# Kernel tuning notes

Measured on AMD Instinct MI355X. Metric: run time of the kernel, lower is better.

## Reference

```python
import jax, jax.numpy as jnp
import numpy as np

B, N, H, DH, ORDER, DEG = 64, 256, 8, 64, 4, 16
D = H * DH
TOTAL = B * N
E = TOTAL * DEG


def setup_inputs() -> dict:
    key = jax.random.key(0)
    ks = jax.random.split(key, 16)
    output = jax.random.normal(ks[0], (N, B, D), dtype=jnp.float32)
    # attention weights: positive, row-normalized like softmax output
    attn = jax.nn.softmax(jax.random.normal(ks[1], (B, H, N, N), dtype=jnp.float32), axis=-1)
    out_each_head = jax.random.normal(ks[2], (B, N, H, DH), dtype=jnp.float32)
    # random graph edges, endpoints within the same graph (global node ids)
    g = jax.random.randint(ks[3], (E,), 0, B)
    s = g * N + jax.random.randint(ks[4], (E,), 0, N)
    d = g * N + jax.random.randint(ks[5], (E,), 0, N)
    edge_index = jnp.stack([s, d], axis=0).astype(jnp.int64)
    # full graphs, no padding: feature_indices[:,0]=graph id, [:,1]=node pos
    fi = jnp.stack([jnp.repeat(jnp.arange(B), N), jnp.tile(jnp.arange(N), B)], axis=1).astype(jnp.int64)
    batch = fi[:, 0]
    sc = 0.1
    params = dict(
        W_gcn=jax.random.normal(ks[6], (ORDER, ORDER)) * sc,
        b_gcn=jnp.zeros((ORDER,), jnp.float32),
        W_lin=jax.random.normal(ks[7], (ORDER, ORDER)) * sc,
        b_lin=jnp.zeros((ORDER,), jnp.float32),
        W_cheb=jax.random.normal(ks[8], (ORDER, DH, DH)) * sc,
        b_cheb=jnp.zeros((DH,), jnp.float32),
        W_cat=jax.random.normal(ks[9], (2 * D, D)) * sc,
        b_cat=jnp.zeros((D,), jnp.float32),
        gamma=jnp.ones((D,), jnp.float32),
        beta=jnp.zeros((D,), jnp.float32),
    )
    return dict(output=output, attn=attn, out_each_head=out_each_head,
                edge_index=edge_index, feature_indices=fi, batch=batch, **params)


def reference(output, attn, out_each_head, edge_index, feature_indices, batch,
              W_gcn, b_gcn, W_lin, b_lin, W_cheb, b_cheb, W_cat, b_cat, gamma, beta):
    Bn, Hn, Nn, _ = attn.shape
    C = W_gcn.shape[0]
    total = Bn * Nn
    NT = Hn * total

    # ---- get_filter_coefficients: GCN over fully-connected attention graphs ----
    # edge weights are detached in the original (edge_weight.detach())
    A = jax.lax.stop_gradient(attn).transpose(1, 0, 2, 3).reshape(Hn * Bn, Nn, Nn)
    A_hat = A + jnp.eye(Nn, dtype=A.dtype)  # add self loops (weight 1)
    deg = A_hat.sum(axis=1)                 # deg_j = sum_i A_hat[i,j]
    dinv = jnp.where(deg > 0, jax.lax.rsqrt(deg), 0.0)  # (HB, N)
    # x = ones, so x @ W_gcn is a constant row = column sums of W_gcn
    w_row = W_gcn.sum(axis=0)               # (C,)
    s = jnp.einsum('bi,bij->bj', dinv, A_hat) * dinv     # (HB, N)
    x_c = jnp.tanh(s[:, :, None] * w_row + b_gcn)        # (HB, N, C)
    gap = x_c.mean(axis=1)                  # global avg pool per graph (HB, C)
    coeff = gap @ W_lin + b_lin             # (HB, C) rows ordered (head, batch)

    # ---- dynamic Chebyshev filtering per head on the input graph ----
    offsets = (jnp.arange(Hn) * total).astype(edge_index.dtype)
    src = (edge_index[0][None, :] + offsets[:, None]).reshape(-1)
    dst = (edge_index[1][None, :] + offsets[:, None]).reshape(-1)
    deg_n = jax.ops.segment_sum(jnp.ones(src.shape[0], jnp.float32), dst, num_segments=NT)
    dinv_n = jnp.where(deg_n > 0, jax.lax.rsqrt(deg_n), 0.0)
    norm_e = -(dinv_n[src] * dinv_n[dst])   # scaled Laplacian L_hat = -D^-1/2 A D^-1/2

    def prop(x):  # L_hat @ x via gather/scatter
        return jax.ops.segment_sum(norm_e[:, None] * x[src], dst, num_segments=NT)

    # nodes ordered (head, batch, node)
    x0 = out_each_head.transpose(2, 0, 1, 3).reshape(NT, DH)
    batch_all = (batch[None, :] + (jnp.arange(Hn) * Bn)[:, None]).reshape(-1)  # graph id h*B+b
    c_node = coeff[batch_all]               # (NT, ORDER) per-node dynamic coefficients

    T_prev, T_cur = x0, prop(x0)
    acc = c_node[:, 0:1] * (T_prev @ W_cheb[0]) + c_node[:, 1:2] * (T_cur @ W_cheb[1])
    for k in range(2, C):
        T_next = 2.0 * prop(T_cur) - T_prev
        acc = acc + c_node[:, k:k + 1] * (T_next @ W_cheb[k])
        T_prev, T_cur = T_cur, T_next
    acc = acc + b_cheb                      # (NT, DH)

    # regroup heads: (H, B*N, DH) -> (B*N, H*DH), scatter back to (N, B, D)
    filtered = acc.reshape(Hn, total, DH).transpose(1, 0, 2).reshape(total, Hn * DH)
    out_filtered = jnp.zeros_like(output).at[feature_indices[:, 1], feature_indices[:, 0], :].set(filtered)

    # skip connection + linear_cat + final LayerNorm
    out_cat = jnp.concatenate([output, out_filtered], axis=-1)
    out = out_cat @ W_cat + b_cat
    mu = out.mean(axis=-1, keepdims=True)
    var = ((out - mu) ** 2).mean(axis=-1, keepdims=True)
    out = (out - mu) * jax.lax.rsqrt(var + 1e-5) * gamma + beta
    return out
```

## Files before the change

kernel.cpp:

```cpp
#include <hip/hip_runtime.h>
#include <stdint.h>

#define Bq      64
#define Nq      256
#define Hq      8
#define DHq     64
#define TOTALq  16384
#define NTq     131072
#define Dq      512

typedef __attribute__((ext_vector_type(8))) short short8;
typedef __attribute__((ext_vector_type(4))) float floatx4;

__device__ __forceinline__ unsigned short f2bf(float f) {
    union { float f; unsigned int u; } c; c.f = f;
    unsigned int u = c.u;
    return (unsigned short)((u + 0x7fffu + ((u >> 16) & 1u)) >> 16);
}
__device__ __forceinline__ float bf2f(unsigned short u) {
    union { unsigned int u; float f; } c; c.u = ((unsigned int)u) << 16;
    return c.f;
}


__global__ void count_deg_kernel(const int* __restrict__ dstp, int* __restrict__ cnt, int E) {
    int e = blockIdx.x * 256 + threadIdx.x;
    if (e < E) atomicAdd(&cnt[dstp[e]], 1);
}

__global__ void dinv_kernel(const int* __restrict__ cnt, float* __restrict__ dinv_n) {
    int v = blockIdx.x * 256 + threadIdx.x;
    if (v < TOTALq) {
        int c = cnt[v];
        dinv_n[v] = (c > 0) ? rsqrtf((float)c) : 0.0f;
    }
}

__global__ void pscatter_kernel(const int* __restrict__ srcp, const int* __restrict__ dstp,
                                const float* __restrict__ dinv_n, float* __restrict__ Pf, int E) {
    int e = blockIdx.x * 256 + threadIdx.x;
    if (e >= E) return;
    int s = srcp[e], d = dstp[e];
    int g = d >> 8;
    atomicAdd(&Pf[((size_t)g << 16) + ((size_t)(d & 255) << 8) + (s & 255)],
              -(dinv_n[s] * dinv_n[d]));
}

__global__ void pconv_kernel(const float* __restrict__ Pf, unsigned short* __restrict__ Pb) {
    int i = (blockIdx.x * 256 + threadIdx.x) * 4;
    float4 v = *(const float4*)(Pf + i);
    unsigned int lo = (unsigned int)f2bf(v.x) | ((unsigned int)f2bf(v.y) << 16);
    unsigned int hi = (unsigned int)f2bf(v.z) | ((unsigned int)f2bf(v.w) << 16);
    *(uint2*)(Pb + i) = make_uint2(lo, hi);
}

__global__ void x0t_kernel(const float* __restrict__ X, unsigned short* __restrict__ Xt) {
    __shared__ float tile[64 * 68];
    int t = threadIdx.x;
    int n0 = blockIdx.x * 64, c0 = blockIdx.y * 64;
#pragma unroll
    for (int it = 0; it < 4; ++it) {
        int idx = it * 256 + t;
        int nr = idx >> 4, sub = idx & 15;
        float4 v = *(const float4*)(X + (size_t)(n0 + nr) * 512 + c0 + sub * 4);
        *(float4*)(&tile[nr * 68 + sub * 4]) = v;
    }
    __syncthreads();
#pragma unroll
    for (int it = 0; it < 2; ++it) {
        int idx = it * 256 + t;
        int cr = idx >> 3, sub = idx & 7;
        unsigned int pk[4];
#pragma unroll
        for (int q = 0; q < 4; ++q) {
            unsigned short a = f2bf(tile[(sub * 8 + q * 2 + 0) * 68 + cr]);
            unsigned short b = f2bf(tile[(sub * 8 + q * 2 + 1) * 68 + cr]);
            pk[q] = (unsigned int)a | ((unsigned int)b << 16);
        }
        *(uint4*)(Xt + (size_t)(c0 + cr) * 16384 + n0 + sub * 8) =
            make_uint4(pk[0], pk[1], pk[2], pk[3]);
    }
}

__global__ void wchebt_kernel(const float* __restrict__ W, float* __restrict__ WT) {
    int idx = blockIdx.x * 256 + threadIdx.x;
    int k = idx >> 12, rem = idx & 4095;
    int n = rem >> 6, j = rem & 63;
    WT[idx] = W[(k << 12) + (j << 6) + n];
}

__global__ __launch_bounds__(512)
void coeff_kernel(const float* __restrict__ attn,
                  const float* __restrict__ Wg, const float* __restrict__ bg,
                  const float* __restrict__ Wlin, const float* __restrict__ blin,
                  float* __restrict__ coeff) {
    __shared__ floatx4 part[8][64];
    __shared__ floatx4 dinv4[64];
    const int g = blockIdx.x;
    const int h = g >> 6;
    const int b = g & 63;
    const float* A = attn + ((size_t)(b * Hq + h)) * (Nq * Nq);
    const int tid = threadIdx.x;
    const int rg = tid >> 6;
    const int cv = tid & 63;
    const float* Ap = A + cv * 4;

    floatx4 s1 = (floatx4){0.f, 0.f, 0.f, 0.f};
#pragma unroll 8
    for (int r = 0; r < 32; ++r)
        s1 += *(const floatx4*)(Ap + (size_t)(rg * 32 + r) * 256);
    part[rg][cv] = s1;
    __syncthreads();

    if (tid < 64) {
        floatx4 cs = part[0][tid];
#pragma unroll
        for (int i = 1; i < 8; ++i) cs += part[i][tid];
        floatx4 dv;
#pragma unroll
        for (int i = 0; i < 4; ++i) dv[i] = rsqrtf(cs[i] + 1.0f);
        dinv4[tid] = dv;
    }
    __syncthreads();

    const float* dsc = (const float*)dinv4;
    floatx4 s2 = (floatx4){0.f, 0.f, 0.f, 0.f};
#pragma unroll 8
    for (int r = 0; r < 32; ++r) {
        int rr = rg * 32 + r;
        s2 += dsc[rr] * (*(const floatx4*)(Ap + (size_t)rr * 256));
    }
    part[rg][cv] = s2;
    __syncthreads();

    if (tid < 64) {
        floatx4 ws = part[0][tid];
#pragma unroll
        for (int i = 1; i < 8; ++i) ws += part[i][tid];
        floatx4 dv = dinv4[tid];
        floatx4 sj = (ws + dv) * dv;

        float wr[4], bgl[4];
#pragma unroll
        for (int c = 0; c < 4; ++c) {
            wr[c]  = Wg[0 * 4 + c] + Wg[1 * 4 + c] + Wg[2 * 4 + c] + Wg[3 * 4 + c];
            bgl[c] = bg[c];
        }
        float v[4];
#pragma unroll
        for (int c = 0; c < 4; ++c) {
            v[c] = tanhf(sj[0] * wr[c] + bgl[c]) + tanhf(sj[1] * wr[c] + bgl[c]) +
                   tanhf(sj[2] * wr[c] + bgl[c]) + tanhf(sj[3] * wr[c] + bgl[c]);
#pragma unroll
            for (int o = 32; o >= 1; o >>= 1) v[c] += __shfl_down(v[c], o, 64);
        }
        float g0 = __shfl(v[0], 0, 64), g1 = __shfl(v[1], 0, 64);
        float g2 = __shfl(v[2], 0, 64), g3 = __shfl(v[3], 0, 64);
        if (tid < 4) {
            float r = blin[tid] + (g0 * Wlin[0 * 4 + tid] + g1 * Wlin[1 * 4 + tid] +
                                   g2 * Wlin[2 * 4 + tid] + g3 * Wlin[3 * 4 + tid]) *
                                      (1.0f / 256.0f);
            coeff[g * 4 + tid] = r;
        }
    }
}

__global__ __launch_bounds__(256, 2)
void cheb_prop(const unsigned short* __restrict__ Pb,
               const unsigned short* __restrict__ Tc,
               const unsigned short* __restrict__ Tp,
               unsigned short* __restrict__ Tn, int first) {
    __shared__ unsigned short A_lds[128 * 40];
    __shared__ unsigned short B_lds[128 * 40];
    const int b = blockIdx.x, mb = blockIdx.y, cb = blockIdx.z;
    const int tid = threadIdx.x, lane = tid & 63, wv = tid >> 6;
    const int wr = wv & 1, wc = wv >> 1, quad = lane >> 4, l15 = lane & 15;
    const unsigned short* Pbase = Pb + ((size_t)b << 16) + (size_t)mb * 128 * 256;

    floatx4 acc[4][4];
#pragma unroll
    for (int rt = 0; rt < 4; ++rt)
#pragma unroll
        for (int ct = 0; ct < 4; ++ct) acc[rt][ct] = (floatx4){0.f, 0.f, 0.f, 0.f};

    for (int kt = 0; kt < 8; ++kt) {
        const int kc = kt * 32;
        __syncthreads();
#pragma unroll
        for (int it = 0; it < 2; ++it) {
            int idx = it * 256 + tid;
            int row = idx >> 2, sub = idx & 3;
            *(uint4*)(A_lds + row * 40 + sub * 8) =
                *(const uint4*)(Pbase + row * 256 + kc + sub * 8);
            *(uint4*)(B_lds + row * 40 + sub * 8) =
                *(const uint4*)(Tc + (size_t)(cb * 128 + row) * 16384 + b * 256 + kc + sub * 8);
        }
        __syncthreads();
        short8 af[4], bfr[4];
#pragma unroll
        for (int rt = 0; rt < 4; ++rt)
            af[rt] = *(const short8*)(A_lds + (wr * 64 + rt * 16 + l15) * 40 + quad * 8);
#pragma unroll
        for (int ct = 0; ct < 4; ++ct)
            bfr[ct] = *(const short8*)(B_lds + (wc * 64 + ct * 16 + l15) * 40 + quad * 8);
#pragma unroll
        for (int rt = 0; rt < 4; ++rt)
#pragma unroll
            for (int ct = 0; ct < 4; ++ct)
                acc[rt][ct] = __builtin_amdgcn_mfma_f32_16x16x32_bf16(af[rt], bfr[ct],
                                                                     acc[rt][ct], 0, 0, 0);
    }
#pragma unroll
    for (int rt = 0; rt < 4; ++rt)
#pragma unroll
        for (int ct = 0; ct < 4; ++ct) {
            int col = cb * 128 + wc * 64 + ct * 16 + l15;
            int m = mb * 128 + wr * 64 + rt * 16 + quad * 4;
            size_t base = (size_t)col * 16384 + b * 256 + m;
            float v[4];
            if (first) {
#pragma unroll
                for (int i = 0; i < 4; ++i) v[i] = acc[rt][ct][i];
            } else {
                uint2 tp = *(const uint2*)(Tp + base);
                v[0] = 2.0f * acc[rt][ct][0] - bf2f((unsigned short)(tp.x & 0xffff));
                v[1] = 2.0f * acc[rt][ct][1] - bf2f((unsigned short)(tp.x >> 16));
                v[2] = 2.0f * acc[rt][ct][2] - bf2f((unsigned short)(tp.y & 0xffff));
                v[3] = 2.0f * acc[rt][ct][3] - bf2f((unsigned short)(tp.y >> 16));
            }
            unsigned int lo = (unsigned int)f2bf(v[0]) | ((unsigned int)f2bf(v[1]) << 16);
            unsigned int hi = (unsigned int)f2bf(v[2]) | ((unsigned int)f2bf(v[3]) << 16);
            *(uint2*)(Tn + base) = make_uint2(lo, hi);
        }
}

__global__ __launch_bounds__(256, 2)
void filt_kernel(const float* __restrict__ oeh,
                 const unsigned short* __restrict__ T1t, const unsigned short* __restrict__ T2t,
                 const unsigned short* __restrict__ T3t, const float* __restrict__ WchTf,
                 const float* __restrict__ coeff, const float* __restrict__ bch,
                 unsigned short* __restrict__ filtb) {
    __shared__ unsigned short A_lds[256 * 72];
    __shared__ unsigned short W_lds[64 * 72];
    const int b = blockIdx.x, h = blockIdx.y;
    const int tid = threadIdx.x, lane = tid & 63, wv = tid >> 6;
    const int quad = lane >> 4, l15 = lane & 15;

    floatx4 acc[4][4];
#pragma unroll
    for (int rt = 0; rt < 4; ++rt)
#pragma unroll
        for (int ct = 0; ct < 4; ++ct) acc[rt][ct] = (floatx4){0.f, 0.f, 0.f, 0.f};

    for (int k = 0; k < 4; ++k) {
        float ck = coeff[(h * Bq + b) * 4 + k];
        __syncthreads();
        if (k == 0) {
#pragma unroll
            for (int it = 0; it < 8; ++it) {
                int idx = it * 256 + tid;
                int row = idx >> 3, sub = idx & 7;
                const float* sp = oeh + (size_t)(b * 256 + row) * 512 + h * 64 + sub * 8;
                float4 v0 = *(const float4*)sp;
                float4 v1 = *(const float4*)(sp + 4);
                unsigned int p0 = (unsigned int)f2bf(v0.x) | ((unsigned int)f2bf(v0.y) << 16);
                unsigned int p1 = (unsigned int)f2bf(v0.z) | ((unsigned int)f2bf(v0.w) << 16);
                unsigned int p2 = (unsigned int)f2bf(v1.x) | ((unsigned int)f2bf(v1.y) << 16);
                unsigned int p3 = (unsigned int)f2bf(v1.z) | ((unsigned int)f2bf(v1.w) << 16);
                *(uint4*)(A_lds + row * 72 + ((sub ^ ((row >> 3) & 7)) << 3)) =
                    make_uint4(p0, p1, p2, p3);
            }
        } else {
            const unsigned short* Tk = (k == 1) ? T1t : (k == 2) ? T2t : T3t;
            const unsigned short* base = Tk + (size_t)(h * 64) * 16384 + b * 256;
#pragma unroll
            for (int it = 0; it < 4; ++it) {
                int idx = it * 256 + tid;
                int cr2 = idx >> 5;
                int nch = idx & 31;
                int n0 = nch * 8;
                int crA = cr2 * 2;
                uint4 a  = *(const uint4*)(base + (size_t)crA * 16384 + n0);
                uint4 c4 = *(const uint4*)(base + (size_t)(crA + 1) * 16384 + n0);
                unsigned swz = (unsigned)((((crA >> 3) ^ (nch & 7)) << 3) + (crA & 7));
                unsigned short* dst = A_lds + swz;
                unsigned av[4] = {a.x, a.y, a.z, a.w};
                unsigned cv4[4] = {c4.x, c4.y, c4.z, c4.w};
#pragma unroll
                for (int w2 = 0; w2 < 4; ++w2) {
                    unsigned lo = (av[w2] & 0xffffu) | (cv4[w2] << 16);
                    unsigned hi = (av[w2] >> 16) | (cv4[w2] & 0xffff0000u);
                    *(unsigned*)(dst + (n0 + w2 * 2 + 0) * 72) = lo;
                    *(unsigned*)(dst + (n0 + w2 * 2 + 1) * 72) = hi;
                }
            }
        }
#pragma unroll
        for (int it = 0; it < 2; ++it) {
            int idx = it * 256 + tid;
            int r = idx >> 3, sub = idx & 7;
            const float* wp = WchTf + k * 4096 + r * 64 + sub * 8;
            float4 w0 = *(const float4*)wp;
            float4 w1 = *(const float4*)(wp + 4);
            unsigned int p0 = (unsigned int)f2bf(w0.x * ck) | ((unsigned int)f2bf(w0.y * ck) << 16);
            unsigned int p1 = (unsigned int)f2bf(w0.z * ck) | ((unsigned int)f2bf(w0.w * ck) << 16);
            unsigned int p2 = (unsigned int)f2bf(w1.x * ck) | ((unsigned int)f2bf(w1.y * ck) << 16);
            unsigned int p3 = (unsigned int)f2bf(w1.z * ck) | ((unsigned int)f2bf(w1.w * ck) << 16);
            *(uint4*)(W_lds + r * 72 + sub * 8) = make_uint4(p0, p1, p2, p3);
        }
        __syncthreads();
#pragma unroll
        for (int kk = 0; kk < 2; ++kk) {
            short8 af[4], bfr[4];
#pragma unroll
            for (int rt = 0; rt < 4; ++rt) {
                int node = wv * 64 + rt * 16 + l15;
                int blk = ((kk << 2) + quad) ^ ((node >> 3) & 7);
                af[rt] = *(const short8*)(A_lds + node * 72 + (blk << 3));
            }
#pragma unroll
            for (int ct = 0; ct < 4; ++ct)
                bfr[ct] = *(const short8*)(W_lds + (ct * 16 + l15) * 72 + kk * 32 + quad * 8);
#pragma unroll
            for (int rt = 0; rt < 4; ++rt)
#pragma unroll
                for (int ct = 0; ct < 4; ++ct)
                    acc[rt][ct] = __builtin_amdgcn_mfma_f32_16x16x32_bf16(af[rt], bfr[ct],
                                                                         acc[rt][ct], 0, 0, 0);
        }
    }
#pragma unroll
    for (int rt = 0; rt < 4; ++rt)
#pragma unroll
        for (int ct = 0; ct < 4; ++ct) {
            int coln = ct * 16 + l15;
            float bias = bch[coln];
#pragma unroll
            for (int i = 0; i < 4; ++i) {
                int m = wv * 64 + rt * 16 + quad * 4 + i;
                size_t r = (size_t)m * 64 + b;
                filtb[r * 512 + h * 64 + coln] = f2bf(acc[rt][ct][i] + bias);
            }
        }
}

__global__ void wt2_kernel(const float* __restrict__ W, unsigned short* __restrict__ Wt2) {
    int idx = blockIdx.x * 256 + threadIdx.x;
    int col = idx & 511;
    int ktq = idx >> 9;
    const float* src = W + (size_t)(ktq * 8) * 512 + col;
    unsigned int pk[4];
#pragma unroll
    for (int q2 = 0; q2 < 4; ++q2) {
        unsigned short a = f2bf(src[(q2 * 2 + 0) * 512]);
        unsigned short b = f2bf(src[(q2 * 2 + 1) * 512]);
        pk[q2] = (unsigned int)a | ((unsigned int)b << 16);
    }
    *(uint4*)(Wt2 + (size_t)idx * 8) = make_uint4(pk[0], pk[1], pk[2], pk[3]);
}

__global__ __launch_bounds__(512, 2)
void gemm_ln_mfma(const float* __restrict__ outp, const unsigned short* __restrict__ filtb,
                  const unsigned short* __restrict__ Wt2, const float* __restrict__ bcat,
                  const float* __restrict__ gamma, const float* __restrict__ beta,
                  float* __restrict__ out) {
    extern __shared__ unsigned char smc[];
    unsigned short* A_lds0 = (unsigned short*)smc;
    unsigned short* A_lds1 = (unsigned short*)(smc + 4096);
    float* ep = (float*)smc;

    const int tid = threadIdx.x;
    const int lane = tid & 63;
    const int wv = tid >> 6;
    const int quad = lane >> 4;
    const int l15 = lane & 15;
    const int r0 = blockIdx.x * 64;

    const int s_row = tid >> 3;
    const int s_sub = tid & 7;
    const int s_q   = s_sub >> 1;
    const int s_e   = (s_sub & 1) * 4;

    const size_t boff = (size_t)(quad * 512 + wv * 64 + l15) * 8;

    floatx4 acc[4][4];
#pragma unroll
    for (int rt = 0; rt < 4; ++rt)
#pragma unroll
        for (int ct = 0; ct < 4; ++ct) acc[rt][ct] = (floatx4){0.f, 0.f, 0.f, 0.f};

    short8 bA[4], bB[4];

    {
#pragma unroll
        for (int ct = 0; ct < 4; ++ct)
            bA[ct] = *(const short8*)(Wt2 + boff + ct * 128);
        float4 av = *(const float4*)(outp + (size_t)(r0 + s_row) * 512 + s_sub * 4);
        uint2 ap;
        ap.x = (unsigned int)f2bf(av.x) | ((unsigned int)f2bf(av.y) << 16);
        ap.y = (unsigned int)f2bf(av.z) | ((unsigned int)f2bf(av.w) << 16);
        *(uint2*)(A_lds0 + (s_q * 64 + s_row) * 8 + s_e) = ap;
        __syncthreads();
    }

#define GSTEP(KT, BC, BN, AC, AN, HASNEXT)                                          \
    do {                                                                            \
        const int kt_ = (KT);                                                       \
        const bool hn_ = (HASNEXT);                                                 \
        const bool isf_ = (kt_ + 1 < 16);                                           \
        float4 av_; uint2 afb_;                                                     \
        if (hn_) {                                                                  \
            _Pragma("unroll")                                                       \
            for (int ct = 0; ct < 4; ++ct)                                          \
                BN[ct] = *(const short8*)(Wt2 + (size_t)(kt_ + 1) * 16384 +         \
                                          boff + ct * 128);                         \
            const int kc_ = (kt_ + 1) * 32;                                         \
            if (isf_)                                                               \
                av_ = *(const float4*)(outp + (size_t)(r0 + s_row) * 512 +          \
                                       kc_ + s_sub * 4);                            \
            else                                                                    \
                afb_ = *(const uint2*)(filtb + (size_t)(r0 + s_row) * 512 +         \
                                       (kc_ - 512) + s_sub * 4);                    \
        }                                                                           \
        short8 af_[4];                                                              \
        _Pragma("unroll")                                                           \
        for (int rt = 0; rt < 4; ++rt)                                              \
            af_[rt] = *(const short8*)(AC + (quad * 64 + rt * 16 + l15) * 8);       \
        _Pragma("unroll")                                                           \
        for (int rt = 0; rt < 4; ++rt)                                              \
            _Pragma("unroll")                                                       \
            for (int ct = 0; ct < 4; ++ct)                                          \
                acc[rt][ct] = __builtin_amdgcn_mfma_f32_16x16x32_bf16(              \
                    af_[rt], BC[ct], acc[rt][ct], 0, 0, 0);                         \
        if (hn_) {                                                                  \
            uint2 ap_;                                                              \
            if (isf_) {                                                             \
                ap_.x = (unsigned int)f2bf(av_.x) | ((unsigned int)f2bf(av_.y) << 16); \
                ap_.y = (unsigned int)f2bf(av_.z) | ((unsigned int)f2bf(av_.w) << 16); \
            } else {                                                                \
                ap_ = afb_;                                                         \
            }                                                                       \
            *(uint2*)(AN + (s_q * 64 + s_row) * 8 + s_e) = ap_;                     \
        }                                                                           \
        __syncthreads();                                                            \
    } while (0)

    for (int kt2 = 0; kt2 < 16; ++kt2) {
        GSTEP(2 * kt2,     bA, bB, A_lds0, A_lds1, true);
        GSTEP(2 * kt2 + 1, bB, bA, A_lds1, A_lds0, kt2 < 15);
    }
#undef GSTEP

    float gg[8], bb[8];
#pragma unroll
    for (int i = 0; i < 8; ++i) { gg[i] = gamma[i * 64 + lane]; bb[i] = beta[i * 64 + lane]; }
    float bc[4];
#pragma unroll
    for (int ct = 0; ct < 4; ++ct) bc[ct] = bcat[wv * 64 + ct * 16 + l15];

    for (int half = 0; half < 2; ++half) {
        __syncthreads();
#pragma unroll
        for (int rt2 = 0; rt2 < 2; ++rt2) {
            const int rt = half * 2 + rt2;
#pragma unroll
            for (int ct = 0; ct < 4; ++ct) {
                const int col = wv * 64 + ct * 16 + l15;
#pragma unroll
                for (int i = 0; i < 4; ++i) {
                    const int row_l = rt2 * 16 + quad * 4 + i;
                    ep[row_l * 512 + col] = acc[rt][ct][i] + bc[ct];
                }
            }
        }
        __syncthreads();
#pragma unroll
        for (int m4 = 0; m4 < 4; ++m4) {
            const int m = wv * 4 + m4;
            float s = 0.0f, ss = 0.0f;
#pragma unroll
            for (int i = 0; i < 8; ++i) {
                float v = ep[m * 512 + i * 64 + lane];
                s += v; ss += v * v;
            }
#pragma unroll
            for (int o = 32; o >= 1; o >>= 1) {
                s += __shfl_down(s, o, 64);
                ss += __shfl_down(ss, o, 64);
            }
            s = __shfl(s, 0, 64);
            ss = __shfl(ss, 0, 64);
            const float mu = s * (1.0f / 512.0f);
            const float var = ss * (1.0f / 512.0f) - mu * mu;
            const float rs = rsqrtf(var + 1e-5f);
            const int r = r0 + half * 32 + m;
#pragma unroll
            for (int i = 0; i < 8; ++i) {
                const int d = i * 64 + lane;
                out[(size_t)r * 512 + d] = (ep[m * 512 + d] - mu) * rs * gg[i] + bb[i];
            }
        }
    }
}

extern "C" void kernel_launch(void* const* d_in, const int* in_sizes, int n_in,
                              void* d_out, int out_size, void* d_ws, size_t ws_size,
                              hipStream_t stream) {
    const float* output       = (const float*)d_in[0];
    const float* attn         = (const float*)d_in[1];
    const float* oeh          = (const float*)d_in[2];
    const int*   edge_index   = (const int*)d_in[3];
    const float* W_gcn        = (const float*)d_in[6];
    const float* b_gcn        = (const float*)d_in[7];
    const float* W_lin        = (const float*)d_in[8];
    const float* b_lin        = (const float*)d_in[9];
    const float* W_cheb       = (const float*)d_in[10];
    const float* b_cheb       = (const float*)d_in[11];
    const float* W_cat        = (const float*)d_in[12];
    const float* b_cat        = (const float*)d_in[13];
    const float* gamma        = (const float*)d_in[14];
    const float* beta         = (const float*)d_in[15];
    float* out = (float*)d_out;

    const int E = in_sizes[3] / 2;
    const int* srcp = edge_index;
    const int* dstp = edge_index + E;

    uint8_t* ws = (uint8_t*)d_ws;
    size_t cur = 0;
    auto alloc = [&](size_t bytes) -> void* {
        void* p = ws + cur;
        cur += (bytes + 255) & ~(size_t)255;
        return p;
    };
    int*   cnt     = (int*)alloc(TOTALq * sizeof(int));
    float* dinv_n  = (float*)alloc(TOTALq * sizeof(float));
    float* Pf      = (float*)alloc((size_t)64 * 65536 * sizeof(float));
    unsigned short* Pb   = (unsigned short*)alloc((size_t)64 * 65536 * 2);
    float* coeff   = (float*)alloc(512 * 4 * sizeof(float));
    unsigned short* X0_t = (unsigned short*)alloc((size_t)512 * 16384 * 2);
    unsigned short* T1_t = (unsigned short*)alloc((size_t)512 * 16384 * 2);
    unsigned short* T2_t = (unsigned short*)alloc((size_t)512 * 16384 * 2);
    unsigned short* T3_t = (unsigned short*)alloc((size_t)512 * 16384 * 2);
    float* WchTf   = (float*)alloc(4 * 64 * 64 * sizeof(float));
    unsigned short* Wt2  = (unsigned short*)alloc((size_t)Dq * 1024 * 2);
    unsigned short* filtb = (unsigned short*)alloc((size_t)TOTALq * Dq * 2);
    (void)ws_size; (void)n_in; (void)out_size;

    hipMemsetAsync(cnt, 0, TOTALq * sizeof(int), stream);
    count_deg_kernel<<<(E + 255) / 256, 256, 0, stream>>>(dstp, cnt, E);
    dinv_kernel<<<TOTALq / 256, 256, 0, stream>>>(cnt, dinv_n);
    hipMemsetAsync(Pf, 0, (size_t)64 * 65536 * sizeof(float), stream);
    pscatter_kernel<<<(E + 255) / 256, 256, 0, stream>>>(srcp, dstp, dinv_n, Pf, E);
    pconv_kernel<<<4096, 256, 0, stream>>>(Pf, Pb);

    x0t_kernel<<<dim3(256, 8), 256, 0, stream>>>(oeh, X0_t);
    coeff_kernel<<<Hq * Bq, 512, 0, stream>>>(attn, W_gcn, b_gcn, W_lin, b_lin, coeff);
    wt2_kernel<<<256, 256, 0, stream>>>(W_cat, Wt2);
    wchebt_kernel<<<64, 256, 0, stream>>>(W_cheb, WchTf);

    dim3 pg(64, 2, 4);
    cheb_prop<<<pg, 256, 0, stream>>>(Pb, X0_t, nullptr, T1_t, 1);
    cheb_prop<<<pg, 256, 0, stream>>>(Pb, T1_t, X0_t, T2_t, 0);
    cheb_prop<<<pg, 256, 0, stream>>>(Pb, T2_t, T1_t, T3_t, 0);

    filt_kernel<<<dim3(64, 8), 256, 0, stream>>>(oeh, T1_t, T2_t, T3_t, WchTf, coeff,
                                                 b_cheb, filtb);

    gemm_ln_mfma<<<TOTALq / 64, 512, 65536, stream>>>(output, filtb, Wt2, b_cat,
                                                      gamma, beta, out);
}
```

Baseline: 437.0 us.

## Fuse Chebyshev propagation and filter GEMM into one per-graph-head kernel

Replaces the transpose kernel, three cheb_prop launches and filt_kernel with a single kernel, one block per (head, graph). Each block keeps its 256x64 slice of T_k resident in LDS in both row- and column-major swizzled layouts. It runs the three propagation GEMMs and the coefficient-scaled W_cheb GEMM on chip, so the T1/T2/T3 intermediates never round-trip through global memory. The P operand is now read straight from global per wave rather than staged in LDS. With 512 blocks of 512 threads and about 73KB of dynamic LDS each, occupancy is reduced.

```diff
diff --git a/kernel.cpp b/kernel.cpp
--- a/kernel.cpp
+++ b/kernel.cpp
@@ -52,34 +52,6 @@
     unsigned int lo = (unsigned int)f2bf(v.x) | ((unsigned int)f2bf(v.y) << 16);
     unsigned int hi = (unsigned int)f2bf(v.z) | ((unsigned int)f2bf(v.w) << 16);
     *(uint2*)(Pb + i) = make_uint2(lo, hi);
-}
-
-__global__ void x0t_kernel(const float* __restrict__ X, unsigned short* __restrict__ Xt) {
-    __shared__ float tile[64 * 68];
-    int t = threadIdx.x;
-    int n0 = blockIdx.x * 64, c0 = blockIdx.y * 64;
-#pragma unroll
-    for (int it = 0; it < 4; ++it) {
-        int idx = it * 256 + t;
-        int nr = idx >> 4, sub = idx & 15;
-        float4 v = *(const float4*)(X + (size_t)(n0 + nr) * 512 + c0 + sub * 4);
-        *(float4*)(&tile[nr * 68 + sub * 4]) = v;
-    }
-    __syncthreads();
-#pragma unroll
-    for (int it = 0; it < 2; ++it) {
-        int idx = it * 256 + t;
-        int cr = idx >> 3, sub = idx & 7;
-        unsigned int pk[4];
-#pragma unroll
-        for (int q = 0; q < 4; ++q) {
-            unsigned short a = f2bf(tile[(sub * 8 + q * 2 + 0) * 68 + cr]);
-            unsigned short b = f2bf(tile[(sub * 8 + q * 2 + 1) * 68 + cr]);
-            pk[q] = (unsigned int)a | ((unsigned int)b << 16);
-        }
-        *(uint4*)(Xt + (size_t)(c0 + cr) * 16384 + n0 + sub * 8) =
-            make_uint4(pk[0], pk[1], pk[2], pk[3]);
-    }
 }
 
 __global__ void wchebt_kernel(const float* __restrict__ W, float* __restrict__ WT) {
@@ -165,181 +137,182 @@
     }
 }
 
-__global__ __launch_bounds__(256, 2)
-void cheb_prop(const unsigned short* __restrict__ Pb,
-               const unsigned short* __restrict__ Tc,
-               const unsigned short* __restrict__ Tp,
-               unsigned short* __restrict__ Tn, int first) {
-    __shared__ unsigned short A_lds[128 * 40];
-    __shared__ unsigned short B_lds[128 * 40];
-    const int b = blockIdx.x, mb = blockIdx.y, cb = blockIdx.z;
-    const int tid = threadIdx.x, lane = tid & 63, wv = tid >> 6;
-    const int wr = wv & 1, wc = wv >> 1, quad = lane >> 4, l15 = lane & 15;
-    const unsigned short* Pbase = Pb + ((size_t)b << 16) + (size_t)mb * 128 * 256;
-
-    floatx4 acc[4][4];
+__global__ __launch_bounds__(512, 2)
+void cheb_fused(const unsigned short* __restrict__ Pb, const float* __restrict__ oeh,
+                const float* __restrict__ WchTf, const float* __restrict__ coeff,
+                const float* __restrict__ bch, unsigned short* __restrict__ filtb) {
+    extern __shared__ unsigned char sm[];
+    unsigned short* cm = (unsigned short*)sm;
+    unsigned short* rm = (unsigned short*)(sm + 32768);
+    unsigned short* Wl = (unsigned short*)(sm + 65536);
+
+    const int g = blockIdx.x;
+    const int b = (g & 7) * 8 + ((g >> 3) & 7);
+    const int h = g >> 6;
+    const int tid = threadIdx.x;
+    const int lane = tid & 63, wv = tid >> 6;
+    const int wr = wv >> 1, wc = wv & 1;
+    const int quad = lane >> 4, l15 = lane & 15;
+
+    const unsigned short* Pbase = Pb + ((size_t)b << 16);
+    const float* cf = coeff + (h * 64 + b) * 4;
+
+    {
+        const int sn = tid >> 1;
+        const int sh = (tid & 1) * 32;
+        const float* sp = oeh + (size_t)(b * 256 + sn) * 512 + h * 64 + sh;
+        unsigned int pk[16];
+#pragma unroll
+        for (int j = 0; j < 8; ++j) {
+            float4 v = *(const float4*)(sp + j * 4);
+            pk[2 * j]     = (unsigned)f2bf(v.x) | ((unsigned)f2bf(v.y) << 16);
+            pk[2 * j + 1] = (unsigned)f2bf(v.z) | ((unsigned)f2bf(v.w) << 16);
+        }
+#pragma unroll
+        for (int jj = 0; jj < 4; ++jj)
+            *(uint4*)(rm + sn * 64 + ((((sh >> 3) + jj) ^ (sn & 7)) << 3)) =
+                make_uint4(pk[4 * jj], pk[4 * jj + 1], pk[4 * jj + 2], pk[4 * jj + 3]);
+#pragma unroll
+        for (int e = 0; e < 32; ++e) {
+            int c = sh + e;
+            unsigned short v =
+                (unsigned short)((e & 1) ? (pk[e >> 1] >> 16) : (pk[e >> 1] & 0xffffu));
+            cm[c * 256 + (((sn >> 3) ^ (c & 31)) << 3) + (sn & 7)] = v;
+        }
+        float ck = cf[0];
+        int r = tid >> 3, su = tid & 7;
+        const float* wp = WchTf + r * 64 + su * 8;
+        float4 w0 = *(const float4*)wp, w1 = *(const float4*)(wp + 4);
+        *(uint4*)(Wl + r * 72 + su * 8) = make_uint4(
+            (unsigned)f2bf(w0.x * ck) | ((unsigned)f2bf(w0.y * ck) << 16),
+            (unsigned)f2bf(w0.z * ck) | ((unsigned)f2bf(w0.w * ck) << 16),
+            (unsigned)f2bf(w1.x * ck) | ((unsigned)f2bf(w1.y * ck) << 16),
+            (unsigned)f2bf(w1.z * ck) | ((unsigned)f2bf(w1.w * ck) << 16));
+    }
+    __syncthreads();
+
+    unsigned int curp[4][2][2], prvp[4][2][2];
 #pragma unroll
     for (int rt = 0; rt < 4; ++rt)
 #pragma unroll
-        for (int ct = 0; ct < 4; ++ct) acc[rt][ct] = (floatx4){0.f, 0.f, 0.f, 0.f};
-
-    for (int kt = 0; kt < 8; ++kt) {
-        const int kc = kt * 32;
-        __syncthreads();
-#pragma unroll
-        for (int it = 0; it < 2; ++it) {
-            int idx = it * 256 + tid;
-            int row = idx >> 2, sub = idx & 3;
-            *(uint4*)(A_lds + row * 40 + sub * 8) =
-                *(const uint4*)(Pbase + row * 256 + kc + sub * 8);
-            *(uint4*)(B_lds + row * 40 + sub * 8) =
-                *(const uint4*)(Tc + (size_t)(cb * 128 + row) * 16384 + b * 256 + kc + sub * 8);
-        }
-        __syncthreads();
-        short8 af[4], bfr[4];
-#pragma unroll
-        for (int rt = 0; rt < 4; ++rt)
-            af[rt] = *(const short8*)(A_lds + (wr * 64 + rt * 16 + l15) * 40 + quad * 8);
-#pragma unroll
-        for (int ct = 0; ct < 4; ++ct)
-            bfr[ct] = *(const short8*)(B_lds + (wc * 64 + ct * 16 + l15) * 40 + quad * 8);
-#pragma unroll
-        for (int rt = 0; rt < 4; ++rt)
-#pragma unroll
-            for (int ct = 0; ct < 4; ++ct)
-                acc[rt][ct] = __builtin_amdgcn_mfma_f32_16x16x32_bf16(af[rt], bfr[ct],
-                                                                     acc[rt][ct], 0, 0, 0);
-    }
+        for (int ct = 0; ct < 2; ++ct)
+#pragma unroll
+            for (int p = 0; p < 2; ++p) {
+                int m = wr * 64 + rt * 16 + quad * 4 + 2 * p;
+                int c = wc * 32 + ct * 16 + l15;
+                curp[rt][ct][p] = *(const unsigned int*)(cm + c * 256 +
+                                                         (((m >> 3) ^ (c & 31)) << 3) + (m & 7));
+                prvp[rt][ct][p] = 0u;
+            }
+
+    floatx4 accf[4][2];
 #pragma unroll
     for (int rt = 0; rt < 4; ++rt)
 #pragma unroll
-        for (int ct = 0; ct < 4; ++ct) {
-            int col = cb * 128 + wc * 64 + ct * 16 + l15;
-            int m = mb * 128 + wr * 64 + rt * 16 + quad * 4;
-            size_t base = (size_t)col * 16384 + b * 256 + m;
-            float v[4];
-            if (first) {
-#pragma unroll
-                for (int i = 0; i < 4; ++i) v[i] = acc[rt][ct][i];
-            } else {
-                uint2 tp = *(const uint2*)(Tp + base);
-                v[0] = 2.0f * acc[rt][ct][0] - bf2f((unsigned short)(tp.x & 0xffff));
-                v[1] = 2.0f * acc[rt][ct][1] - bf2f((unsigned short)(tp.x >> 16));
-                v[2] = 2.0f * acc[rt][ct][2] - bf2f((unsigned short)(tp.y & 0xffff));
-                v[3] = 2.0f * acc[rt][ct][3] - bf2f((unsigned short)(tp.y >> 16));
-            }
-            unsigned int lo = (unsigned int)f2bf(v[0]) | ((unsigned int)f2bf(v[1]) << 16);
-            unsigned int hi = (unsigned int)f2bf(v[2]) | ((unsigned int)f2bf(v[3]) << 16);
-            *(uint2*)(Tn + base) = make_uint2(lo, hi);
-        }
-}
-
-__global__ __launch_bounds__(256, 2)
-void filt_kernel(const float* __restrict__ oeh,
-                 const unsigned short* __restrict__ T1t, const unsigned short* __restrict__ T2t,
-                 const unsigned short* __restrict__ T3t, const float* __restrict__ WchTf,
-                 const float* __restrict__ coeff, const float* __restrict__ bch,
-                 unsigned short* __restrict__ filtb) {
-    __shared__ unsigned short A_lds[256 * 72];
-    __shared__ unsigned short W_lds[64 * 72];
-    const int b = blockIdx.x, h = blockIdx.y;
-    const int tid = threadIdx.x, lane = tid & 63, wv = tid >> 6;
-    const int quad = lane >> 4, l15 = lane & 15;
-
-    floatx4 acc[4][4];
+        for (int ct = 0; ct < 2; ++ct) accf[rt][ct] = (floatx4){0.f, 0.f, 0.f, 0.f};
+
+#pragma unroll
+    for (int k = 0; k < 4; ++k) {
+#pragma unroll
+        for (int kk = 0; kk < 2; ++kk) {
+            short8 af[4], bfw[2];
+#pragma unroll
+            for (int rt = 0; rt < 4; ++rt) {
+                int row = wr * 64 + rt * 16 + l15;
+                af[rt] = *(const short8*)(rm + row * 64 + (((kk * 4 + quad) ^ (row & 7)) << 3));
+            }
+#pragma unroll
+            for (int ct = 0; ct < 2; ++ct) {
+                int oc = wc * 32 + ct * 16 + l15;
+                bfw[ct] = *(const short8*)(Wl + oc * 72 + kk * 32 + quad * 8);
+            }
+#pragma unroll
+            for (int rt = 0; rt < 4; ++rt)
+#pragma unroll
+                for (int ct = 0; ct < 2; ++ct)
+                    accf[rt][ct] = __builtin_amdgcn_mfma_f32_16x16x32_bf16(
+                        af[rt], bfw[ct], accf[rt][ct], 0, 0, 0);
+        }
+        if (k < 3) {
+            floatx4 accp[4][2];
+#pragma unroll
+            for (int rt = 0; rt < 4; ++rt)
+#pragma unroll
+                for (int ct = 0; ct < 2; ++ct) accp[rt][ct] = (floatx4){0.f, 0.f, 0.f, 0.f};
+#pragma unroll
+            for (int kt = 0; kt < 8; ++kt) {
+                short8 ap[4], bp[2];
+#pragma unroll
+                for (int rt = 0; rt < 4; ++rt) {
+                    int row = wr * 64 + rt * 16 + l15;
+                    ap[rt] = *(const short8*)(Pbase + row * 256 + kt * 32 + quad * 8);
+                }
+#pragma unroll
+                for (int ct = 0; ct < 2; ++ct) {
+                    int c = wc * 32 + ct * 16 + l15;
+                    bp[ct] = *(const short8*)(cm + c * 256 + (((kt * 4 + quad) ^ (c & 31)) << 3));
+                }
+#pragma unroll
+                for (int rt = 0; rt < 4; ++rt)
+#pragma unroll
+                    for (int ct = 0; ct < 2; ++ct)
+                        accp[rt][ct] = __builtin_amdgcn_mfma_f32_16x16x32_bf16(
+                            ap[rt], bp[ct], accp[rt][ct], 0, 0, 0);
+            }
+            __syncthreads();
+#pragma unroll
+            for (int rt = 0; rt < 4; ++rt)
+#pragma unroll
+                for (int ct = 0; ct < 2; ++ct)
+#pragma unroll
+                    for (int p = 0; p < 2; ++p) {
+                        float a0 = accp[rt][ct][2 * p], a1 = accp[rt][ct][2 * p + 1];
+                        if (k > 0) {
+                            unsigned pv = prvp[rt][ct][p];
+                            a0 = 2.0f * a0 - bf2f((unsigned short)(pv & 0xffffu));
+                            a1 = 2.0f * a1 - bf2f((unsigned short)(pv >> 16));
+                        }
+                        unsigned nv = (unsigned)f2bf(a0) | ((unsigned)f2bf(a1) << 16);
+                        prvp[rt][ct][p] = curp[rt][ct][p];
+                        curp[rt][ct][p] = nv;
+                        int m = wr * 64 + rt * 16 + quad * 4 + 2 * p;
+                        int c = wc * 32 + ct * 16 + l15;
+                        if (k < 2)
+                            *(unsigned int*)(cm + c * 256 + (((m >> 3) ^ (c & 31)) << 3) +
+                                             (m & 7)) = nv;
+                        rm[m * 64 + (((c >> 3) ^ (m & 7)) << 3) + (c & 7)] =
+                            (unsigned short)(nv & 0xffffu);
+                        rm[(m + 1) * 64 + (((c >> 3) ^ ((m + 1) & 7)) << 3) + (c & 7)] =
+                            (unsigned short)(nv >> 16);
+                    }
+            {
+                float ck = cf[k + 1];
+                int r = tid >> 3, su = tid & 7;
+                const float* wp = WchTf + (k + 1) * 4096 + r * 64 + su * 8;
+                float4 w0 = *(const float4*)wp, w1 = *(const float4*)(wp + 4);
+                *(uint4*)(Wl + r * 72 + su * 8) = make_uint4(
+                    (unsigned)f2bf(w0.x * ck) | ((unsigned)f2bf(w0.y * ck) << 16),
+                    (unsigned)f2bf(w0.z * ck) | ((unsigned)f2bf(w0.w * ck) << 16),
+                    (unsigned)f2bf(w1.x * ck) | ((unsigned)f2bf(w1.y * ck) << 16),
+                    (unsigned)f2bf(w1.z * ck) | ((unsigned)f2bf(w1.w * ck) << 16));
+            }
+            __syncthreads();
+        }
+    }
+
+    float bias[2];
+#pragma unroll
+    for (int ct = 0; ct < 2; ++ct) bias[ct] = bch[wc * 32 + ct * 16 + l15];
 #pragma unroll
     for (int rt = 0; rt < 4; ++rt)
 #pragma unroll
-        for (int ct = 0; ct < 4; ++ct) acc[rt][ct] = (floatx4){0.f, 0.f, 0.f, 0.f};
-
-    for (int k = 0; k < 4; ++k) {
-        float ck = coeff[(h * Bq + b) * 4 + k];
-        __syncthreads();
-        if (k == 0) {
-#pragma unroll
-            for (int it = 0; it < 8; ++it) {
-                int idx = it * 256 + tid;
-                int row = idx >> 3, sub = idx & 7;
-                const float* sp = oeh + (size_t)(b * 256 + row) * 512 + h * 64 + sub * 8;
-                float4 v0 = *(const float4*)sp;
-                float4 v1 = *(const float4*)(sp + 4);
-                unsigned int p0 = (unsigned int)f2bf(v0.x) | ((unsigned int)f2bf(v0.y) << 16);
-                unsigned int p1 = (unsigned int)f2bf(v0.z) | ((unsigned int)f2bf(v0.w) << 16);
-                unsigned int p2 = (unsigned int)f2bf(v1.x) | ((unsigned int)f2bf(v1.y) << 16);
-                unsigned int p3 = (unsigned int)f2bf(v1.z) | ((unsigned int)f2bf(v1.w) << 16);
-                *(uint4*)(A_lds + row * 72 + ((sub ^ ((row >> 3) & 7)) << 3)) =
-                    make_uint4(p0, p1, p2, p3);
-            }
-        } else {
-            const unsigned short* Tk = (k == 1) ? T1t : (k == 2) ? T2t : T3t;
-            const unsigned short* base = Tk + (size_t)(h * 64) * 16384 + b * 256;
-#pragma unroll
-            for (int it = 0; it < 4; ++it) {
-                int idx = it * 256 + tid;
-                int cr2 = idx >> 5;
-                int nch = idx & 31;
-                int n0 = nch * 8;
-                int crA = cr2 * 2;
-                uint4 a  = *(const uint4*)(base + (size_t)crA * 16384 + n0);
-                uint4 c4 = *(const uint4*)(base + (size_t)(crA + 1) * 16384 + n0);
-                unsigned swz = (unsigned)((((crA >> 3) ^ (nch & 7)) << 3) + (crA & 7));
-                unsigned short* dst = A_lds + swz;
-                unsigned av[4] = {a.x, a.y, a.z, a.w};
-                unsigned cv4[4] = {c4.x, c4.y, c4.z, c4.w};
-#pragma unroll
-                for (int w2 = 0; w2 < 4; ++w2) {
-                    unsigned lo = (av[w2] & 0xffffu) | (cv4[w2] << 16);
-                    unsigned hi = (av[w2] >> 16) | (cv4[w2] & 0xffff0000u);
-                    *(unsigned*)(dst + (n0 + w2 * 2 + 0) * 72) = lo;
-                    *(unsigned*)(dst + (n0 + w2 * 2 + 1) * 72) = hi;
-                }
-            }
-        }
-#pragma unroll
-        for (int it = 0; it < 2; ++it) {
-            int idx = it * 256 + tid;
-            int r = idx >> 3, sub = idx & 7;
-            const float* wp = WchTf + k * 4096 + r * 64 + sub * 8;
-            float4 w0 = *(const float4*)wp;
-            float4 w1 = *(const float4*)(wp + 4);
-            unsigned int p0 = (unsigned int)f2bf(w0.x * ck) | ((unsigned int)f2bf(w0.y * ck) << 16);
-            unsigned int p1 = (unsigned int)f2bf(w0.z * ck) | ((unsigned int)f2bf(w0.w * ck) << 16);
-            unsigned int p2 = (unsigned int)f2bf(w1.x * ck) | ((unsigned int)f2bf(w1.y * ck) << 16);
-            unsigned int p3 = (unsigned int)f2bf(w1.z * ck) | ((unsigned int)f2bf(w1.w * ck) << 16);
-            *(uint4*)(W_lds + r * 72 + sub * 8) = make_uint4(p0, p1, p2, p3);
-        }
-        __syncthreads();
-#pragma unroll
-        for (int kk = 0; kk < 2; ++kk) {
-            short8 af[4], bfr[4];
-#pragma unroll
-            for (int rt = 0; rt < 4; ++rt) {
-                int node = wv * 64 + rt * 16 + l15;
-                int blk = ((kk << 2) + quad) ^ ((node >> 3) & 7);
-                af[rt] = *(const short8*)(A_lds + node * 72 + (blk << 3));
-            }
-#pragma unroll
-            for (int ct = 0; ct < 4; ++ct)
-                bfr[ct] = *(const short8*)(W_lds + (ct * 16 + l15) * 72 + kk * 32 + quad * 8);
-#pragma unroll
-            for (int rt = 0; rt < 4; ++rt)
-#pragma unroll
-                for (int ct = 0; ct < 4; ++ct)
-                    acc[rt][ct] = __builtin_amdgcn_mfma_f32_16x16x32_bf16(af[rt], bfr[ct],
-                                                                         acc[rt][ct], 0, 0, 0);
-        }
-    }
-#pragma unroll
-    for (int rt = 0; rt < 4; ++rt)
-#pragma unroll
-        for (int ct = 0; ct < 4; ++ct) {
-            int coln = ct * 16 + l15;
-            float bias = bch[coln];
+        for (int ct = 0; ct < 2; ++ct) {
+            int c = wc * 32 + ct * 16 + l15;
 #pragma unroll
             for (int i = 0; i < 4; ++i) {
-                int m = wv * 64 + rt * 16 + quad * 4 + i;
-                size_t r = (size_t)m * 64 + b;
-                filtb[r * 512 + h * 64 + coln] = f2bf(acc[rt][ct][i] + bias);
+                int m = wr * 64 + rt * 16 + quad * 4 + i;
+                filtb[((size_t)m * 64 + b) * 512 + h * 64 + c] =
+                    f2bf(accf[rt][ct][i] + bias[ct]);
             }
         }
 }
@@ -538,10 +511,6 @@
     float* Pf      = (float*)alloc((size_t)64 * 65536 * sizeof(float));
     unsigned short* Pb   = (unsigned short*)alloc((size_t)64 * 65536 * 2);
     float* coeff   = (float*)alloc(512 * 4 * sizeof(float));
-    unsigned short* X0_t = (unsigned short*)alloc((size_t)512 * 16384 * 2);
-    unsigned short* T1_t = (unsigned short*)alloc((size_t)512 * 16384 * 2);
-    unsigned short* T2_t = (unsigned short*)alloc((size_t)512 * 16384 * 2);
-    unsigned short* T3_t = (unsigned short*)alloc((size_t)512 * 16384 * 2);
     float* WchTf   = (float*)alloc(4 * 64 * 64 * sizeof(float));
     unsigned short* Wt2  = (unsigned short*)alloc((size_t)Dq * 1024 * 2);
     unsigned short* filtb = (unsigned short*)alloc((size_t)TOTALq * Dq * 2);
@@ -554,18 +523,11 @@
     pscatter_kernel<<<(E + 255) / 256, 256, 0, stream>>>(srcp, dstp, dinv_n, Pf, E);
     pconv_kernel<<<4096, 256, 0, stream>>>(Pf, Pb);
 
-    x0t_kernel<<<dim3(256, 8), 256, 0, stream>>>(oeh, X0_t);
     coeff_kernel<<<Hq * Bq, 512, 0, stream>>>(attn, W_gcn, b_gcn, W_lin, b_lin, coeff);
     wt2_kernel<<<256, 256, 0, stream>>>(W_cat, Wt2);
     wchebt_kernel<<<64, 256, 0, stream>>>(W_cheb, WchTf);
 
-    dim3 pg(64, 2, 4);
-    cheb_prop<<<pg, 256, 0, stream>>>(Pb, X0_t, nullptr, T1_t, 1);
-    cheb_prop<<<pg, 256, 0, stream>>>(Pb, T1_t, X0_t, T2_t, 0);
-    cheb_prop<<<pg, 256, 0, stream>>>(Pb, T2_t, T1_t, T3_t, 0);
-
-    filt_kernel<<<dim3(64, 8), 256, 0, stream>>>(oeh, T1_t, T2_t, T3_t, WchTf, coeff,
-                                                 b_cheb, filtb);
+    cheb_fused<<<512, 512, 74752, stream>>>(Pb, oeh, WchTf, coeff, b_cheb, filtb);
 
     gemm_ln_mfma<<<TOTALq / 64, 512, 65536, stream>>>(output, filtb, Wt2, b_cat,
                                                       gamma, beta, out);
```

After: 414.4 us. -5.2%, faster.
